# Optimization experiments

Measured on AMD Instinct MI355X. Metric: run time of the kernel, lower is better.

Reference implementation:

```python
import jax, jax.numpy as jnp
import numpy as np

NUM_GRAPHS = 1000


def setup_inputs() -> dict:
    key = jax.random.key(0)
    ks = jax.random.split(key, 8)
    N, E, F_IN, H = 100000, 1600000, 128, 64
    x = jax.random.normal(ks[0], (N, F_IN), dtype=jnp.float32)
    edge_index = jax.random.randint(ks[1], (2, E), 0, N, dtype=jnp.int64)
    batch = jnp.sort(jax.random.randint(ks[2], (N,), 0, NUM_GRAPHS, dtype=jnp.int64))
    # Glorot-ish scaled weights
    W1 = jax.random.normal(ks[3], (F_IN, H), dtype=jnp.float32) / np.sqrt(F_IN)
    W2 = jax.random.normal(ks[4], (H, H), dtype=jnp.float32) / np.sqrt(H)
    W3 = jax.random.normal(ks[5], (H, H), dtype=jnp.float32) / np.sqrt(H)
    Wl = jax.random.normal(ks[6], (H, 1), dtype=jnp.float32) / np.sqrt(H)
    return {
        "x": x, "edge_index": edge_index, "batch": batch,
        "W1": W1, "b1": jnp.zeros((H,), jnp.float32),
        "W2": W2, "b2": jnp.zeros((H,), jnp.float32),
        "W3": W3, "b3": jnp.zeros((H,), jnp.float32),
        "Wl": Wl, "bl": jnp.zeros((1,), jnp.float32),
    }


def _gcn_prep(edge_index, n_nodes):
    """Add self-loops and compute symmetric normalization coefficients."""
    loops = jnp.arange(n_nodes, dtype=edge_index.dtype)
    src = jnp.concatenate([edge_index[0], loops])  # [E+N]
    dst = jnp.concatenate([edge_index[1], loops])  # [E+N]
    deg = jax.ops.segment_sum(jnp.ones_like(dst, dtype=jnp.float32), dst,
                              num_segments=n_nodes)
    dinv = jnp.where(deg > 0, jax.lax.rsqrt(jnp.maximum(deg, 1.0)), 0.0)
    norm = dinv[src] * dinv[dst]  # [E+N]
    return src, dst, norm


def _gcn_conv(h, W, b, src, dst, norm, n_nodes):
    h = h @ W                              # [N, H] linear transform first
    msg = h[src] * norm[:, None]           # gather + normalize
    agg = jax.ops.segment_sum(msg, dst, num_segments=n_nodes)  # scatter-add
    return agg + b


def reference(x, edge_index, batch, W1, b1, W2, b2, W3, b3, Wl, bl):
    n_nodes = x.shape[0]
    src, dst, norm = _gcn_prep(edge_index, n_nodes)
    h = jax.nn.relu(_gcn_conv(x, W1, b1, src, dst, norm, n_nodes))
    h = jax.nn.relu(_gcn_conv(h, W2, b2, src, dst, norm, n_nodes))
    h = _gcn_conv(h, W3, b3, src, dst, norm, n_nodes)
    # global_mean_pool over graphs
    sums = jax.ops.segment_sum(h, batch, num_segments=NUM_GRAPHS)
    cnts = jax.ops.segment_sum(jnp.ones((n_nodes,), jnp.float32), batch,
                               num_segments=NUM_GRAPHS)
    pooled = sums / jnp.maximum(cnts, 1.0)[:, None]
    # dropout is identity in eval mode
    return pooled @ Wl + bl
```

## Files before the change

### kernel.cpp

```cpp
#include <hip/hip_runtime.h>
#include <stdint.h>

#define BKT 1024
#define EPB 4096

typedef __attribute__((ext_vector_type(8))) __bf16 bf16x8;
typedef __attribute__((ext_vector_type(4))) float floatx4;

__device__ __forceinline__ float bf2f(unsigned short h) {
    return __uint_as_float(((unsigned)h) << 16);
}
__device__ __forceinline__ float4 bf4(ushort4 v) {
    return make_float4(bf2f(v.x), bf2f(v.y), bf2f(v.z), bf2f(v.w));
}
__device__ __forceinline__ unsigned short f2bf(float f) {
    unsigned u = __float_as_uint(f);
    u = u + 0x7FFFu + ((u >> 16) & 1u);
    return (unsigned short)(u >> 16);
}
__device__ __forceinline__ ushort4 pack4(float a, float b, float c, float d) {
    ushort4 r; r.x = f2bf(a); r.y = f2bf(b); r.z = f2bf(c); r.w = f2bf(d); return r;
}


__global__ void w3l_kernel(const float* __restrict__ W3, const float* __restrict__ Wl,
                           float* __restrict__ w3l) {
    int k = threadIdx.x;
    float s = 0.f;
#pragma unroll 16
    for (int c = 0; c < 64; ++c) s += W3[k * 64 + c] * Wl[c];
    w3l[k] = s;
}


__global__ __launch_bounds__(256) void coarse_hist(const int* __restrict__ dst,
                                                   int* __restrict__ coarse, int E, int NBK) {
    __shared__ int h[128];
    if (threadIdx.x < 128) h[threadIdx.x] = 0;
    __syncthreads();
    int stride = gridDim.x * 256;
    int gid = blockIdx.x * 256 + threadIdx.x;
    const int4* d4 = (const int4*)dst;
    int E4 = E >> 2;
    for (int i = gid; i < E4; i += stride) {
        int4 v = d4[i];
        atomicAdd(&h[v.x >> 10], 1);
        atomicAdd(&h[v.y >> 10], 1);
        atomicAdd(&h[v.z >> 10], 1);
        atomicAdd(&h[v.w >> 10], 1);
    }
    for (int i = (E4 << 2) + gid; i < E; i += stride)
        atomicAdd(&h[dst[i] >> 10], 1);
    __syncthreads();
    if (threadIdx.x < NBK) {
        int v = h[threadIdx.x];
        if (v) atomicAdd(&coarse[threadIdx.x], v);
    }
}

__global__ void coarse_scan(const int* __restrict__ coarse, int* __restrict__ bbase,
                            int NBK, int E) {
    if (threadIdx.x == 0 && blockIdx.x == 0) {
        int run = 0;
        for (int i = 0; i < NBK; ++i) { bbase[i] = run; run += coarse[i]; }
        bbase[NBK] = E;
    }
}


__global__ __launch_bounds__(256) void partition_kernel(const int* __restrict__ src,
                                                        const int* __restrict__ dst,
                                                        const int* __restrict__ bbase,
                                                        int* __restrict__ gbcur,
                                                        int2* __restrict__ pairs,
                                                        int E, int NBK) {
    __shared__ int2 stage[EPB];
    __shared__ int  hist[128], offs[129], gbase[128], lcur[128];
    int base = blockIdx.x * EPB;
    int cntE = min(EPB, E - base);
    if (threadIdx.x < 128) hist[threadIdx.x] = 0;
    __syncthreads();
    {
        const int4* d4 = (const int4*)(dst + base);
        int c4 = cntE >> 2;
        for (int i = threadIdx.x; i < c4; i += 256) {
            int4 v = d4[i];
            atomicAdd(&hist[v.x >> 10], 1);
            atomicAdd(&hist[v.y >> 10], 1);
            atomicAdd(&hist[v.z >> 10], 1);
            atomicAdd(&hist[v.w >> 10], 1);
        }
        for (int i = (c4 << 2) + (int)threadIdx.x; i < cntE; i += 256)
            atomicAdd(&hist[dst[base + i] >> 10], 1);
    }
    __syncthreads();
    if (threadIdx.x == 0) {
        int run = 0;
        for (int b = 0; b < NBK; ++b) { offs[b] = run; run += hist[b]; }
        offs[NBK] = run;
    }
    __syncthreads();
    if (threadIdx.x < NBK) {
        int b = threadIdx.x;
        int h = hist[b];
        if (h > 0) gbase[b] = bbase[b] + atomicAdd(&gbcur[b << 4], h);
        lcur[b] = offs[b];
    }
    __syncthreads();
    for (int i = threadIdx.x; i < cntE; i += 256) {
        int e = base + i;
        int d = dst[e];
        int b = d >> 10;
        int slot = atomicAdd(&lcur[b], 1);
        stage[slot] = make_int2(src[e], d);
    }
    __syncthreads();
    int total = offs[NBK];
    for (int j = threadIdx.x; j < total; j += 256) {
        int lo = 0, hi = NBK;
        while (lo < hi) { int mid = (lo + hi) >> 1; if (offs[mid + 1] <= j) lo = mid + 1; else hi = mid; }
        pairs[gbase[lo] + (j - offs[lo])] = stage[j];
    }
}


__global__ __launch_bounds__(256) void bucket_build(const int2* __restrict__ pairs,
                                                    const int* __restrict__ bbase,
                                                    int* __restrict__ rowptr,
                                                    int* __restrict__ csr, int N, int E) {
    __shared__ int cnt[BKT];
    __shared__ int psum[256];
    int b = blockIdx.x;
    int nbase = b << 10;
    int pbeg = bbase[b], pend = bbase[b + 1];
    for (int i = threadIdx.x; i < BKT; i += 256) cnt[i] = 0;
    __syncthreads();
    for (int j = pbeg + (int)threadIdx.x; j < pend; j += 256)
        atomicAdd(&cnt[pairs[j].y - nbase], 1);
    __syncthreads();
    int i0 = threadIdx.x * 4;
    int c0 = cnt[i0], c1 = cnt[i0 + 1], c2 = cnt[i0 + 2], c3 = cnt[i0 + 3];
    int local = c0 + c1 + c2 + c3;
    psum[threadIdx.x] = local;
    __syncthreads();
    for (int d = 1; d < 256; d <<= 1) {
        int t = (threadIdx.x >= d) ? psum[threadIdx.x - d] : 0;
        __syncthreads();
        psum[threadIdx.x] += t;
        __syncthreads();
    }
    int excl = psum[threadIdx.x] - local;
    int o0 = pbeg + excl;
    int o1 = o0 + c0, o2 = o1 + c1, o3 = o2 + c2;
    int n0 = nbase + i0;
    if (n0 < N)     rowptr[n0]     = o0;
    if (n0 + 1 < N) rowptr[n0 + 1] = o1;
    if (n0 + 2 < N) rowptr[n0 + 2] = o2;
    if (n0 + 3 < N) rowptr[n0 + 3] = o3;
    cnt[i0] = o0; cnt[i0 + 1] = o1; cnt[i0 + 2] = o2; cnt[i0 + 3] = o3;
    __syncthreads();
    for (int j = pbeg + (int)threadIdx.x; j < pend; j += 256) {
        int2 p = pairs[j];
        int slot = atomicAdd(&cnt[p.y - nbase], 1);
        csr[slot] = p.x;
    }
    if (b == 0 && threadIdx.x == 0) rowptr[N] = E;
}


__global__ __launch_bounds__(256) void gemm1_mfma(const float* __restrict__ X,
                                                  const float* __restrict__ W,
                                                  const int* __restrict__ rowptr,
                                                  __bf16* __restrict__ gbh, int N) {
    __shared__ __align__(16) __bf16 Wt[64][136];
    for (int i = threadIdx.x; i < 128 * 64; i += 256) {
        int k = i >> 6, c = i & 63;
        Wt[c][k] = (__bf16)W[i];
    }
    __syncthreads();

    int wave = threadIdx.x >> 6;
    int l = threadIdx.x & 63;
    int cidx = l & 15;
    int g = l >> 4;
    int wbase = blockIdx.x * 64 + wave * 16;

    int arow = wbase + cidx;
    int arowc = min(arow, N - 1);
    const float4* xr = (const float4*)(X + (size_t)arowc * 128);
    bf16x8 afr[4];
#pragma unroll
    for (int kb = 0; kb < 4; ++kb) {
        float4 p = xr[kb * 8 + g * 2];
        float4 q = xr[kb * 8 + g * 2 + 1];
        bf16x8 a;
        a[0] = (__bf16)p.x; a[1] = (__bf16)p.y; a[2] = (__bf16)p.z; a[3] = (__bf16)p.w;
        a[4] = (__bf16)q.x; a[5] = (__bf16)q.y; a[6] = (__bf16)q.z; a[7] = (__bf16)q.w;
        afr[kb] = a;
    }

    floatx4 acc[4];
#pragma unroll
    for (int ct = 0; ct < 4; ++ct) acc[ct] = (floatx4){0.f, 0.f, 0.f, 0.f};

#pragma unroll
    for (int ct = 0; ct < 4; ++ct) {
#pragma unroll
        for (int kb = 0; kb < 4; ++kb) {
            bf16x8 bfr = *(const bf16x8*)&Wt[ct * 16 + cidx][kb * 32 + g * 8];
            acc[ct] = __builtin_amdgcn_mfma_f32_16x16x32_bf16(afr[kb], bfr, acc[ct], 0, 0, 0);
        }
    }

    int r0 = wbase + g * 4;
    int rp[5];
#pragma unroll
    for (int i = 0; i < 5; ++i) rp[i] = rowptr[min(r0 + i, N)];
#pragma unroll
    for (int i = 0; i < 4; ++i) {
        int row = r0 + i;
        if (row < N) {
            float dv = rsqrtf((float)(rp[i + 1] - rp[i]) + 1.0f);
#pragma unroll
            for (int ct = 0; ct < 4; ++ct)
                gbh[(size_t)row * 64 + ct * 16 + cidx] = (__bf16)(acc[ct][i] * dv);
        }
    }
}


__global__ __launch_bounds__(256) void fused_layer_kernel(const ushort4* __restrict__ gb,
                                                          const int* __restrict__ rowptr,
                                                          const int* __restrict__ csr,
                                                          const float* __restrict__ bias,
                                                          const float* __restrict__ W,
                                                          ushort4* __restrict__ out, int N) {
    __shared__ float Ws[64 * 64];
    __shared__ float T[16][72];
    {
        const float4* Wv = (const float4*)W;
        float4* Wsv = (float4*)Ws;
        for (int i = threadIdx.x; i < 64 * 16; i += 256) Wsv[i] = Wv[i];
    }
    int row = threadIdx.x >> 4;
    int node = blockIdx.x * 16 + row;
    int t = threadIdx.x & 15;
    int c = t * 4;
    float dinv = 0.f;
    if (node < N) {
        int beg = rowptr[node], end = rowptr[node + 1];
        dinv = rsqrtf((float)(end - beg) + 1.0f);
        float4 acc = bf4(gb[(size_t)node * 16 + t]);
        int j = beg;
        for (; j + 8 <= end; j += 8) {
            int s0 = csr[j], s1 = csr[j + 1], s2 = csr[j + 2], s3 = csr[j + 3];
            int s4 = csr[j + 4], s5 = csr[j + 5], s6 = csr[j + 6], s7 = csr[j + 7];
            float4 v0 = bf4(gb[(size_t)s0 * 16 + t]);
            float4 v1 = bf4(gb[(size_t)s1 * 16 + t]);
            float4 v2 = bf4(gb[(size_t)s2 * 16 + t]);
            float4 v3 = bf4(gb[(size_t)s3 * 16 + t]);
            float4 v4 = bf4(gb[(size_t)s4 * 16 + t]);
            float4 v5 = bf4(gb[(size_t)s5 * 16 + t]);
            float4 v6 = bf4(gb[(size_t)s6 * 16 + t]);
            float4 v7 = bf4(gb[(size_t)s7 * 16 + t]);
            acc.x += ((v0.x + v1.x) + (v2.x + v3.x)) + ((v4.x + v5.x) + (v6.x + v7.x));
            acc.y += ((v0.y + v1.y) + (v2.y + v3.y)) + ((v4.y + v5.y) + (v6.y + v7.y));
            acc.z += ((v0.z + v1.z) + (v2.z + v3.z)) + ((v4.z + v5.z) + (v6.z + v7.z));
            acc.w += ((v0.w + v1.w) + (v2.w + v3.w)) + ((v4.w + v5.w) + (v6.w + v7.w));
        }
        for (; j + 2 <= end; j += 2) {
            int s0 = csr[j], s1 = csr[j + 1];
            float4 v0 = bf4(gb[(size_t)s0 * 16 + t]);
            float4 v1 = bf4(gb[(size_t)s1 * 16 + t]);
            acc.x += v0.x + v1.x; acc.y += v0.y + v1.y;
            acc.z += v0.z + v1.z; acc.w += v0.w + v1.w;
        }
        if (j < end) {
            int s0 = csr[j];
            float4 v0 = bf4(gb[(size_t)s0 * 16 + t]);
            acc.x += v0.x; acc.y += v0.y; acc.z += v0.z; acc.w += v0.w;
        }
        float4 bb = *(const float4*)&bias[c];
        T[row][c + 0] = fmaxf(acc.x * dinv + bb.x, 0.f);
        T[row][c + 1] = fmaxf(acc.y * dinv + bb.y, 0.f);
        T[row][c + 2] = fmaxf(acc.z * dinv + bb.z, 0.f);
        T[row][c + 3] = fmaxf(acc.w * dinv + bb.w, 0.f);
    }
    __syncthreads();
    if (node >= N) return;
    float4 o = make_float4(0.f, 0.f, 0.f, 0.f);
#pragma unroll 16
    for (int k = 0; k < 64; ++k) {
        float tv = T[row][k];
        float4 wv = *(const float4*)&Ws[k * 64 + c];
        o.x += tv * wv.x; o.y += tv * wv.y;
        o.z += tv * wv.z; o.w += tv * wv.w;
    }
    out[(size_t)node * 16 + t] = pack4(o.x * dinv, o.y * dinv, o.z * dinv, o.w * dinv);
}


__global__ __launch_bounds__(256) void agg_dot2_kernel(const ushort4* __restrict__ gb,
                                                       const int* __restrict__ rowptr,
                                                       const int* __restrict__ csr,
                                                       const float* __restrict__ bias,
                                                       const float* __restrict__ w3l,
                                                       float* __restrict__ p, int N) {
    int tid = blockIdx.x * blockDim.x + threadIdx.x;
    int node = tid >> 4;
    if (node >= N) return;
    int t = tid & 15;
    int beg = rowptr[node], end = rowptr[node + 1];
    float dinv = rsqrtf((float)(end - beg) + 1.0f);
    float4 acc = bf4(gb[(size_t)node * 16 + t]);
    int j = beg;
    for (; j + 8 <= end; j += 8) {
        int s0 = csr[j], s1 = csr[j + 1], s2 = csr[j + 2], s3 = csr[j + 3];
        int s4 = csr[j + 4], s5 = csr[j + 5], s6 = csr[j + 6], s7 = csr[j + 7];
        float4 v0 = bf4(gb[(size_t)s0 * 16 + t]);
        float4 v1 = bf4(gb[(size_t)s1 * 16 + t]);
        float4 v2 = bf4(gb[(size_t)s2 * 16 + t]);
        float4 v3 = bf4(gb[(size_t)s3 * 16 + t]);
        float4 v4 = bf4(gb[(size_t)s4 * 16 + t]);
        float4 v5 = bf4(gb[(size_t)s5 * 16 + t]);
        float4 v6 = bf4(gb[(size_t)s6 * 16 + t]);
        float4 v7 = bf4(gb[(size_t)s7 * 16 + t]);
        acc.x += ((v0.x + v1.x) + (v2.x + v3.x)) + ((v4.x + v5.x) + (v6.x + v7.x));
        acc.y += ((v0.y + v1.y) + (v2.y + v3.y)) + ((v4.y + v5.y) + (v6.y + v7.y));
        acc.z += ((v0.z + v1.z) + (v2.z + v3.z)) + ((v4.z + v5.z) + (v6.z + v7.z));
        acc.w += ((v0.w + v1.w) + (v2.w + v3.w)) + ((v4.w + v5.w) + (v6.w + v7.w));
    }
    for (; j + 2 <= end; j += 2) {
        int s0 = csr[j], s1 = csr[j + 1];
        float4 v0 = bf4(gb[(size_t)s0 * 16 + t]);
        float4 v1 = bf4(gb[(size_t)s1 * 16 + t]);
        acc.x += v0.x + v1.x; acc.y += v0.y + v1.y;
        acc.z += v0.z + v1.z; acc.w += v0.w + v1.w;
    }
    if (j < end) {
        int s0 = csr[j];
        float4 v0 = bf4(gb[(size_t)s0 * 16 + t]);
        acc.x += v0.x; acc.y += v0.y; acc.z += v0.z; acc.w += v0.w;
    }
    float4 bb = *(const float4*)&bias[t * 4];
    float4 wv = *(const float4*)&w3l[t * 4];
    float hx = fmaxf(acc.x * dinv + bb.x, 0.f);
    float hy = fmaxf(acc.y * dinv + bb.y, 0.f);
    float hz = fmaxf(acc.z * dinv + bb.z, 0.f);
    float hw = fmaxf(acc.w * dinv + bb.w, 0.f);
    float s = (hx * wv.x + hy * wv.y) + (hz * wv.z + hw * wv.w);
    s += __shfl_xor(s, 1);
    s += __shfl_xor(s, 2);
    s += __shfl_xor(s, 4);
    s += __shfl_xor(s, 8);
    if (t == 0) p[node] = s * dinv;
}


__global__ __launch_bounds__(256) void scalar_agg(const float* __restrict__ p,
                                                  const int* __restrict__ rowptr,
                                                  const int* __restrict__ csr,
                                                  float* __restrict__ s_node, int N) {
    int n = blockIdx.x * 256 + threadIdx.x;
    if (n >= N) return;
    int beg = rowptr[n], end = rowptr[n + 1];
    float dinv = rsqrtf((float)(end - beg) + 1.0f);
    float acc = p[n];
    int j = beg;
    for (; j + 4 <= end; j += 4) {
        float a0 = p[csr[j]], a1 = p[csr[j + 1]], a2 = p[csr[j + 2]], a3 = p[csr[j + 3]];
        acc += (a0 + a1) + (a2 + a3);
    }
    for (; j < end; ++j) acc += p[csr[j]];
    s_node[n] = acc * dinv;
}


__device__ __forceinline__ int lower_bound_dev(const int* __restrict__ a, int n, int v) {
    int lo = 0, hi = n;
    while (lo < hi) { int mid = (lo + hi) >> 1; if (a[mid] < v) lo = mid + 1; else hi = mid; }
    return lo;
}

__global__ void pool_out_kernel(const float* __restrict__ s_node, const int* __restrict__ batch,
                                const float* __restrict__ b3, const float* __restrict__ Wl,
                                const float* __restrict__ bl, float* __restrict__ out, int N) {
    float v = b3[threadIdx.x] * Wl[threadIdx.x];
    for (int d = 32; d; d >>= 1) v += __shfl_down(v, d);
    float bldot = __shfl(v, 0, 64);

    int gidx = blockIdx.x;
    int lo = lower_bound_dev(batch, N, gidx);
    int hi = lower_bound_dev(batch, N, gidx + 1);
    float s = 0.f;
    for (int i = lo + threadIdx.x; i < hi; i += 64) s += s_node[i];
    for (int d = 32; d; d >>= 1) s += __shfl_down(s, d);
    if (threadIdx.x == 0)
        out[gidx] = s / fmaxf((float)(hi - lo), 1.0f) + bldot + bl[0];
}


extern "C" void kernel_launch(void* const* d_in, const int* in_sizes, int n_in,
                              void* d_out, int out_size, void* d_ws, size_t ws_size,
                              hipStream_t stream) {
    const float* x   = (const float*)d_in[0];
    const int*   ei  = (const int*)d_in[1];
    const int*   bat = (const int*)d_in[2];
    const float* W1  = (const float*)d_in[3];
    const float* b1  = (const float*)d_in[4];
    const float* W2  = (const float*)d_in[5];
    const float* b2  = (const float*)d_in[6];
    const float* W3  = (const float*)d_in[7];
    const float* b3  = (const float*)d_in[8];
    const float* Wl  = (const float*)d_in[9];
    const float* bl  = (const float*)d_in[10];

    const int N = in_sizes[0] / 128;
    const int E = in_sizes[1] / 2;
    const int G = out_size;

    const int* src = ei;
    const int* dst = ei + E;

    const int NBK = (N + BKT - 1) / BKT;
    const int Np = (N + 4) & ~3;

    int*     rowptr = (int*)d_ws;
    int*     coarse = rowptr + Np;
    int*     bbase  = coarse + 128;
    float*   w3l    = (float*)(bbase + 132);
    int*     gbcur  = (int*)(w3l + 64);
    int*     csr    = gbcur + (size_t)NBK * 16;
    int2*    pairs  = (int2*)(csr + E);
    ushort4* gbA    = (ushort4*)(pairs + E);
    ushort4* gbB    = gbA + (size_t)N * 16;
    float*   pbuf   = (float*)(gbB + (size_t)N * 16);
    float*   s_node = pbuf + N;

    hipMemsetAsync(coarse, 0, (324 + (size_t)NBK * 16) * sizeof(int), stream);
    w3l_kernel<<<1, 64, 0, stream>>>(W3, Wl, w3l);
    coarse_hist<<<256, 256, 0, stream>>>(dst, coarse, E, NBK);
    coarse_scan<<<1, 64, 0, stream>>>(coarse, bbase, NBK, E);
    partition_kernel<<<(E + EPB - 1) / EPB, 256, 0, stream>>>(src, dst, bbase, gbcur, pairs, E, NBK);
    bucket_build<<<NBK, 256, 0, stream>>>(pairs, bbase, rowptr, csr, N, E);

    const int tileGrid = (N + 15) / 16;
    const int aggGrid  = (int)(((size_t)N * 16 + 255) / 256);

    gemm1_mfma<<<(N + 63) / 64, 256, 0, stream>>>(x, W1, rowptr, (__bf16*)gbA, N);
    fused_layer_kernel<<<tileGrid, 256, 0, stream>>>(gbA, rowptr, csr, b1, W2, gbB, N);
    agg_dot2_kernel<<<aggGrid, 256, 0, stream>>>(gbB, rowptr, csr, b2, w3l, pbuf, N);
    scalar_agg<<<(N + 255) / 256, 256, 0, stream>>>(pbuf, rowptr, csr, s_node, N);
    pool_out_kernel<<<G, 64, 0, stream>>>(s_node, bat, b3, Wl, bl, (float*)d_out, N);
}
```

Baseline: 232.4 us.

## Split layer-2 into gather kernel plus MFMA GEMM, pack edge pairs into 32 bits

The fused layer-2 kernel, which did gather, relu and a scalar FP32 64x64 matmul from shared memory, is split into a pure gather+bias+relu kernel that writes bf16 activations and a separate MFMA bf16 GEMM kernel. The aim is to move the dense transform onto matrix cores and free the gather kernel from a large shared-memory tile that limited occupancy. The price is an extra round trip of an N x 64 bf16 buffer through global memory and one more launch. In addition, partition pairs are packed as (src<<10 | dst&1023) in one 32-bit word, halving pair traffic, and EPB is doubled to 8192; the packing assumes src fits in 22 bits.

```diff
diff --git a/kernel.cpp b/kernel.cpp
--- a/kernel.cpp
+++ b/kernel.cpp
@@ -2,7 +2,7 @@
 #include <stdint.h>
 
 #define BKT 1024
-#define EPB 4096
+#define EPB 8192
 
 typedef __attribute__((ext_vector_type(8))) __bf16 bf16x8;
 typedef __attribute__((ext_vector_type(4))) float floatx4;
@@ -72,10 +72,10 @@
                                                         const int* __restrict__ dst,
                                                         const int* __restrict__ bbase,
                                                         int* __restrict__ gbcur,
-                                                        int2* __restrict__ pairs,
+                                                        unsigned* __restrict__ pairs,
                                                         int E, int NBK) {
-    __shared__ int2 stage[EPB];
-    __shared__ int  hist[128], offs[129], gbase[128], lcur[128];
+    __shared__ unsigned stage[EPB];
+    __shared__ int hist[128], offs[129], gbase[128], lcur[128];
     int base = blockIdx.x * EPB;
     int cntE = min(EPB, E - base);
     if (threadIdx.x < 128) hist[threadIdx.x] = 0;
@@ -112,7 +112,7 @@
         int d = dst[e];
         int b = d >> 10;
         int slot = atomicAdd(&lcur[b], 1);
-        stage[slot] = make_int2(src[e], d);
+        stage[slot] = ((unsigned)src[e] << 10) | (unsigned)(d & 1023);
     }
     __syncthreads();
     int total = offs[NBK];
@@ -124,7 +124,7 @@
 }
 
 
-__global__ __launch_bounds__(256) void bucket_build(const int2* __restrict__ pairs,
+__global__ __launch_bounds__(256) void bucket_build(const unsigned* __restrict__ pairs,
                                                     const int* __restrict__ bbase,
                                                     int* __restrict__ rowptr,
                                                     int* __restrict__ csr, int N, int E) {
@@ -136,7 +136,7 @@
     for (int i = threadIdx.x; i < BKT; i += 256) cnt[i] = 0;
     __syncthreads();
     for (int j = pbeg + (int)threadIdx.x; j < pend; j += 256)
-        atomicAdd(&cnt[pairs[j].y - nbase], 1);
+        atomicAdd(&cnt[pairs[j] & 1023u], 1);
     __syncthreads();
     int i0 = threadIdx.x * 4;
     int c0 = cnt[i0], c1 = cnt[i0 + 1], c2 = cnt[i0 + 2], c3 = cnt[i0 + 3];
@@ -160,9 +160,9 @@
     cnt[i0] = o0; cnt[i0 + 1] = o1; cnt[i0 + 2] = o2; cnt[i0 + 3] = o3;
     __syncthreads();
     for (int j = pbeg + (int)threadIdx.x; j < pend; j += 256) {
-        int2 p = pairs[j];
-        int slot = atomicAdd(&cnt[p.y - nbase], 1);
-        csr[slot] = p.x;
+        unsigned p = pairs[j];
+        int slot = atomicAdd(&cnt[p & 1023u], 1);
+        csr[slot] = (int)(p >> 10);
     }
     if (b == 0 && threadIdx.x == 0) rowptr[N] = E;
 }
@@ -229,74 +229,106 @@
 }
 
 
-__global__ __launch_bounds__(256) void fused_layer_kernel(const ushort4* __restrict__ gb,
+__global__ __launch_bounds__(256) void gather_relu_kernel(const ushort4* __restrict__ gb,
                                                           const int* __restrict__ rowptr,
                                                           const int* __restrict__ csr,
                                                           const float* __restrict__ bias,
-                                                          const float* __restrict__ W,
-                                                          ushort4* __restrict__ out, int N) {
-    __shared__ float Ws[64 * 64];
-    __shared__ float T[16][72];
-    {
-        const float4* Wv = (const float4*)W;
-        float4* Wsv = (float4*)Ws;
-        for (int i = threadIdx.x; i < 64 * 16; i += 256) Wsv[i] = Wv[i];
-    }
-    int row = threadIdx.x >> 4;
-    int node = blockIdx.x * 16 + row;
-    int t = threadIdx.x & 15;
-    int c = t * 4;
-    float dinv = 0.f;
-    if (node < N) {
-        int beg = rowptr[node], end = rowptr[node + 1];
-        dinv = rsqrtf((float)(end - beg) + 1.0f);
-        float4 acc = bf4(gb[(size_t)node * 16 + t]);
-        int j = beg;
-        for (; j + 8 <= end; j += 8) {
-            int s0 = csr[j], s1 = csr[j + 1], s2 = csr[j + 2], s3 = csr[j + 3];
-            int s4 = csr[j + 4], s5 = csr[j + 5], s6 = csr[j + 6], s7 = csr[j + 7];
-            float4 v0 = bf4(gb[(size_t)s0 * 16 + t]);
-            float4 v1 = bf4(gb[(size_t)s1 * 16 + t]);
-            float4 v2 = bf4(gb[(size_t)s2 * 16 + t]);
-            float4 v3 = bf4(gb[(size_t)s3 * 16 + t]);
-            float4 v4 = bf4(gb[(size_t)s4 * 16 + t]);
-            float4 v5 = bf4(gb[(size_t)s5 * 16 + t]);
-            float4 v6 = bf4(gb[(size_t)s6 * 16 + t]);
-            float4 v7 = bf4(gb[(size_t)s7 * 16 + t]);
-            acc.x += ((v0.x + v1.x) + (v2.x + v3.x)) + ((v4.x + v5.x) + (v6.x + v7.x));
-            acc.y += ((v0.y + v1.y) + (v2.y + v3.y)) + ((v4.y + v5.y) + (v6.y + v7.y));
-            acc.z += ((v0.z + v1.z) + (v2.z + v3.z)) + ((v4.z + v5.z) + (v6.z + v7.z));
-            acc.w += ((v0.w + v1.w) + (v2.w + v3.w)) + ((v4.w + v5.w) + (v6.w + v7.w));
+                                                          ushort4* __restrict__ h, int N) {
+    int tid = blockIdx.x * blockDim.x + threadIdx.x;
+    int node = tid >> 4;
+    if (node >= N) return;
+    int t = tid & 15;
+    int beg = rowptr[node], end = rowptr[node + 1];
+    float dinv = rsqrtf((float)(end - beg) + 1.0f);
+    float4 acc = bf4(gb[(size_t)node * 16 + t]);
+    int j = beg;
+    for (; j + 8 <= end; j += 8) {
+        int s0 = csr[j], s1 = csr[j + 1], s2 = csr[j + 2], s3 = csr[j + 3];
+        int s4 = csr[j + 4], s5 = csr[j + 5], s6 = csr[j + 6], s7 = csr[j + 7];
+        float4 v0 = bf4(gb[(size_t)s0 * 16 + t]);
+        float4 v1 = bf4(gb[(size_t)s1 * 16 + t]);
+        float4 v2 = bf4(gb[(size_t)s2 * 16 + t]);
+        float4 v3 = bf4(gb[(size_t)s3 * 16 + t]);
+        float4 v4 = bf4(gb[(size_t)s4 * 16 + t]);
+        float4 v5 = bf4(gb[(size_t)s5 * 16 + t]);
+        float4 v6 = bf4(gb[(size_t)s6 * 16 + t]);
+        float4 v7 = bf4(gb[(size_t)s7 * 16 + t]);
+        acc.x += ((v0.x + v1.x) + (v2.x + v3.x)) + ((v4.x + v5.x) + (v6.x + v7.x));
+        acc.y += ((v0.y + v1.y) + (v2.y + v3.y)) + ((v4.y + v5.y) + (v6.y + v7.y));
+        acc.z += ((v0.z + v1.z) + (v2.z + v3.z)) + ((v4.z + v5.z) + (v6.z + v7.z));
+        acc.w += ((v0.w + v1.w) + (v2.w + v3.w)) + ((v4.w + v5.w) + (v6.w + v7.w));
+    }
+    for (; j + 2 <= end; j += 2) {
+        int s0 = csr[j], s1 = csr[j + 1];
+        float4 v0 = bf4(gb[(size_t)s0 * 16 + t]);
+        float4 v1 = bf4(gb[(size_t)s1 * 16 + t]);
+        acc.x += v0.x + v1.x; acc.y += v0.y + v1.y;
+        acc.z += v0.z + v1.z; acc.w += v0.w + v1.w;
+    }
+    if (j < end) {
+        int s0 = csr[j];
+        float4 v0 = bf4(gb[(size_t)s0 * 16 + t]);
+        acc.x += v0.x; acc.y += v0.y; acc.z += v0.z; acc.w += v0.w;
+    }
+    float4 bb = *(const float4*)&bias[t * 4];
+    h[(size_t)node * 16 + t] = pack4(fmaxf(acc.x * dinv + bb.x, 0.f),
+                                     fmaxf(acc.y * dinv + bb.y, 0.f),
+                                     fmaxf(acc.z * dinv + bb.z, 0.f),
+                                     fmaxf(acc.w * dinv + bb.w, 0.f));
+}
+
+
+__global__ __launch_bounds__(256) void gemm64_mfma(const __bf16* __restrict__ H,
+                                                   const float* __restrict__ W,
+                                                   const int* __restrict__ rowptr,
+                                                   __bf16* __restrict__ out, int N) {
+    __shared__ __align__(16) __bf16 Wt[64][72];
+    for (int i = threadIdx.x; i < 64 * 64; i += 256) {
+        int k = i >> 6, c = i & 63;
+        Wt[c][k] = (__bf16)W[i];
+    }
+    __syncthreads();
+
+    int wave = threadIdx.x >> 6;
+    int l = threadIdx.x & 63;
+    int cidx = l & 15;
+    int g = l >> 4;
+    int wbase = blockIdx.x * 64 + wave * 16;
+
+    int arow = wbase + cidx;
+    int arowc = min(arow, N - 1);
+    const bf16x8* hr = (const bf16x8*)(H + (size_t)arowc * 64);
+    bf16x8 afr[2];
+#pragma unroll
+    for (int kb = 0; kb < 2; ++kb) afr[kb] = hr[kb * 4 + g];
+
+    floatx4 acc[4];
+#pragma unroll
+    for (int ct = 0; ct < 4; ++ct) acc[ct] = (floatx4){0.f, 0.f, 0.f, 0.f};
+
+#pragma unroll
+    for (int ct = 0; ct < 4; ++ct) {
+#pragma unroll
+        for (int kb = 0; kb < 2; ++kb) {
+            bf16x8 bfr = *(const bf16x8*)&Wt[ct * 16 + cidx][kb * 32 + g * 8];
+            acc[ct] = __builtin_amdgcn_mfma_f32_16x16x32_bf16(afr[kb], bfr, acc[ct], 0, 0, 0);
         }
-        for (; j + 2 <= end; j += 2) {
-            int s0 = csr[j], s1 = csr[j + 1];
-            float4 v0 = bf4(gb[(size_t)s0 * 16 + t]);
-            float4 v1 = bf4(gb[(size_t)s1 * 16 + t]);
-            acc.x += v0.x + v1.x; acc.y += v0.y + v1.y;
-            acc.z += v0.z + v1.z; acc.w += v0.w + v1.w;
+    }
+
+    int r0 = wbase + g * 4;
+    int rp[5];
+#pragma unroll
+    for (int i = 0; i < 5; ++i) rp[i] = rowptr[min(r0 + i, N)];
+#pragma unroll
+    for (int i = 0; i < 4; ++i) {
+        int row = r0 + i;
+        if (row < N) {
+            float dv = rsqrtf((float)(rp[i + 1] - rp[i]) + 1.0f);
+#pragma unroll
+            for (int ct = 0; ct < 4; ++ct)
+                out[(size_t)row * 64 + ct * 16 + cidx] = (__bf16)(acc[ct][i] * dv);
         }
-        if (j < end) {
-            int s0 = csr[j];
-            float4 v0 = bf4(gb[(size_t)s0 * 16 + t]);
-            acc.x += v0.x; acc.y += v0.y; acc.z += v0.z; acc.w += v0.w;
-        }
-        float4 bb = *(const float4*)&bias[c];
-        T[row][c + 0] = fmaxf(acc.x * dinv + bb.x, 0.f);
-        T[row][c + 1] = fmaxf(acc.y * dinv + bb.y, 0.f);
-        T[row][c + 2] = fmaxf(acc.z * dinv + bb.z, 0.f);
-        T[row][c + 3] = fmaxf(acc.w * dinv + bb.w, 0.f);
-    }
-    __syncthreads();
-    if (node >= N) return;
-    float4 o = make_float4(0.f, 0.f, 0.f, 0.f);
-#pragma unroll 16
-    for (int k = 0; k < 64; ++k) {
-        float tv = T[row][k];
-        float4 wv = *(const float4*)&Ws[k * 64 + c];
-        o.x += tv * wv.x; o.y += tv * wv.y;
-        o.z += tv * wv.z; o.w += tv * wv.w;
-    }
-    out[(size_t)node * 16 + t] = pack4(o.x * dinv, o.y * dinv, o.z * dinv, o.w * dinv);
+    }
 }
 
 
@@ -425,17 +457,18 @@
     const int NBK = (N + BKT - 1) / BKT;
     const int Np = (N + 4) & ~3;
 
-    int*     rowptr = (int*)d_ws;
-    int*     coarse = rowptr + Np;
-    int*     bbase  = coarse + 128;
-    float*   w3l    = (float*)(bbase + 132);
-    int*     gbcur  = (int*)(w3l + 64);
-    int*     csr    = gbcur + (size_t)NBK * 16;
-    int2*    pairs  = (int2*)(csr + E);
-    ushort4* gbA    = (ushort4*)(pairs + E);
-    ushort4* gbB    = gbA + (size_t)N * 16;
-    float*   pbuf   = (float*)(gbB + (size_t)N * 16);
-    float*   s_node = pbuf + N;
+    int*      rowptr = (int*)d_ws;
+    int*      coarse = rowptr + Np;
+    int*      bbase  = coarse + 128;
+    float*    w3l    = (float*)(bbase + 132);
+    int*      gbcur  = (int*)(w3l + 64);
+    int*      csr    = gbcur + (size_t)NBK * 16;
+    unsigned* pairs  = (unsigned*)(csr + E);
+    ushort4*  gbA    = (ushort4*)(pairs + E);
+    ushort4*  gbB    = gbA + (size_t)N * 16;
+    ushort4*  hbuf   = gbB + (size_t)N * 16;
+    float*    pbuf   = (float*)(hbuf + (size_t)N * 16);
+    float*    s_node = pbuf + N;
 
     hipMemsetAsync(coarse, 0, (324 + (size_t)NBK * 16) * sizeof(int), stream);
     w3l_kernel<<<1, 64, 0, stream>>>(W3, Wl, w3l);
@@ -444,11 +477,11 @@
     partition_kernel<<<(E + EPB - 1) / EPB, 256, 0, stream>>>(src, dst, bbase, gbcur, pairs, E, NBK);
     bucket_build<<<NBK, 256, 0, stream>>>(pairs, bbase, rowptr, csr, N, E);
 
-    const int tileGrid = (N + 15) / 16;
-    const int aggGrid  = (int)(((size_t)N * 16 + 255) / 256);
+    const int aggGrid = (int)(((size_t)N * 16 + 255) / 256);
 
     gemm1_mfma<<<(N + 63) / 64, 256, 0, stream>>>(x, W1, rowptr, (__bf16*)gbA, N);
-    fused_layer_kernel<<<tileGrid, 256, 0, stream>>>(gbA, rowptr, csr, b1, W2, gbB, N);
+    gather_relu_kernel<<<aggGrid, 256, 0, stream>>>(gbA, rowptr, csr, b1, hbuf, N);
+    gemm64_mfma<<<(N + 63) / 64, 256, 0, stream>>>((const __bf16*)hbuf, W2, rowptr, (__bf16*)gbB, N);
     agg_dot2_kernel<<<aggGrid, 256, 0, stream>>>(gbB, rowptr, csr, b2, w3l, pbuf, N);
     scalar_agg<<<(N + 255) / 256, 256, 0, stream>>>(pbuf, rowptr, csr, s_node, N);
     pool_out_kernel<<<G, 64, 0, stream>>>(s_node, bat, b3, Wl, bl, (float*)d_out, N);
```

Measured after the change: 244.4 us. 1.05x slower.
